# Performance work log

Hardware: AMD Instinct MI355X
Metric: run time of the kernel (lower is better)

The kernel has to match this reference:

```python
import jax, jax.numpy as jnp
import numpy as np

N = 50000
E = 800000
F_IN = 512
HID = 32
HEADS = 8
CLS = 64
NEG_SLOPE = 0.2
EPS = 1e-16  # PyG softmax denominator epsilon


def setup_inputs() -> dict:
    key = jax.random.key(0)
    ks = jax.random.split(key, 10)
    x = jax.random.normal(ks[0], (N, F_IN), dtype=jnp.float32)
    edge_index = jax.random.randint(ks[1], (2, E), 0, N, dtype=jnp.int64)
    # layer 1: in=F_IN, heads=HEADS, out_per_head=HID, concat
    s1 = 1.0 / np.sqrt(F_IN)
    W1 = jax.random.normal(ks[2], (F_IN, HEADS * HID), dtype=jnp.float32) * s1
    att_src1 = jax.random.normal(ks[3], (HEADS, HID), dtype=jnp.float32) * 0.1
    att_dst1 = jax.random.normal(ks[4], (HEADS, HID), dtype=jnp.float32) * 0.1
    b1 = jnp.zeros((HEADS * HID,), dtype=jnp.float32)
    # layer 2: in=HEADS*HID, heads=1, out=CLS, no concat
    s2 = 1.0 / np.sqrt(HEADS * HID)
    W2 = jax.random.normal(ks[5], (HEADS * HID, CLS), dtype=jnp.float32) * s2
    att_src2 = jax.random.normal(ks[6], (1, CLS), dtype=jnp.float32) * 0.1
    att_dst2 = jax.random.normal(ks[7], (1, CLS), dtype=jnp.float32) * 0.1
    b2 = jnp.zeros((CLS,), dtype=jnp.float32)
    return {"x": x, "edge_index": edge_index,
            "W1": W1, "att_src1": att_src1, "att_dst1": att_dst1, "b1": b1,
            "W2": W2, "att_src2": att_src2, "att_dst2": att_dst2, "b2": b2}


def gat_conv(x, edge_index, W, att_src, att_dst, bias, concat):
    n = x.shape[0]
    heads, c = att_src.shape
    h = (x @ W).reshape(n, heads, c)                       # [N,H,C]
    # add self loops (PyG GATConv default)
    loop = jnp.arange(n, dtype=edge_index.dtype)
    src = jnp.concatenate([edge_index[0], loop])
    dst = jnp.concatenate([edge_index[1], loop])
    a_src = jnp.einsum('nhc,hc->nh', h, att_src)           # [N,H]
    a_dst = jnp.einsum('nhc,hc->nh', h, att_dst)
    e = a_src[src] + a_dst[dst]                            # [E',H]
    e = jax.nn.leaky_relu(e, NEG_SLOPE)
    # segment softmax over destination node
    m = jax.ops.segment_max(e, dst, num_segments=n)
    e = jnp.exp(e - jax.lax.stop_gradient(m)[dst])
    s = jax.ops.segment_sum(e, dst, num_segments=n)
    alpha = e / (s[dst] + EPS)                             # [E',H]
    msg = h[src] * alpha[:, :, None]                       # [E',H,C]
    out = jax.ops.segment_sum(msg, dst, num_segments=n)    # [N,H,C]
    out = out.reshape(n, heads * c) if concat else out.mean(axis=1)
    return out + bias


def reference(x, edge_index, W1, att_src1, att_dst1, b1, W2, att_src2, att_dst2, b2):
    h = gat_conv(x, edge_index, W1, att_src1, att_dst1, b1, concat=True)
    h = jax.nn.relu(h)
    # F.dropout with training=False (eval) is identity
    h = gat_conv(h, edge_index, W2, att_src2, att_dst2, b2, concat=False)
    return jax.nn.log_softmax(h, axis=1)
```

## Files before the change

kernel.cpp:

```cpp
#include <hip/hip_runtime.h>
#include <hip/hip_bf16.h>
#include <stdint.h>

#define F_IN 512
#define HID 32
#define HEADS 8
#define C1 (HEADS*HID)
#define CLS 64
#define NEG 0.2f
#define EPS 1e-16f

typedef __bf16 bf16x8 __attribute__((ext_vector_type(8)));
typedef __bf16 bf16x4 __attribute__((ext_vector_type(4)));
typedef float  f32x4  __attribute__((ext_vector_type(4)));

__device__ __forceinline__ float leaky(float v) { return v > 0.f ? v : NEG * v; }

__device__ __forceinline__ bf16x8 cvt8(float4 a, float4 b) {
  bf16x8 o;
  o[0] = (__bf16)a.x; o[1] = (__bf16)a.y; o[2] = (__bf16)a.z; o[3] = (__bf16)a.w;
  o[4] = (__bf16)b.x; o[5] = (__bf16)b.y; o[6] = (__bf16)b.z; o[7] = (__bf16)b.w;
  return o;
}

__global__ __launch_bounds__(256) void prep(const float* __restrict__ W1,
    const float* __restrict__ W2, const int* __restrict__ ei,
    __bf16* __restrict__ w1t, __bf16* __restrict__ w2t,
    int* __restrict__ deg, int E) {
  const int b = blockIdx.x, t = threadIdx.x;
  if (b < 64) {
    int i = b * 256 + t;
    int o0 = i * 8;
    int c = o0 >> 9, k0 = o0 & 511;
    bf16x8 o;
#pragma unroll
    for (int j = 0; j < 8; j++) o[j] = (__bf16)W1[(size_t)(k0 + j) * C1 + c];
    *(bf16x8*)(w1t + (size_t)o0) = o;
  } else if (b < 72) {
    int i = (b - 64) * 256 + t;
    int o0 = i * 8;
    int c = o0 >> 8, k0 = o0 & 255;
    bf16x8 o;
#pragma unroll
    for (int j = 0; j < 8; j++) o[j] = (__bf16)W2[(size_t)(k0 + j) * CLS + c];
    *(bf16x8*)(w2t + (size_t)o0) = o;
  } else {
    int e = (b - 72) * 256 + t;
    if (e < E) atomicAdd(&deg[ei[E + e]], 1);
  }
}

__global__ __launch_bounds__(256) void scan_k1(const int* __restrict__ deg,
    int* __restrict__ bsum, int N) {
  __shared__ int ws[4];
  const int t = threadIdx.x, lane = t & 63, wid = t >> 6;
  int i = blockIdx.x * 256 + t;
  int v = (i < N) ? deg[i] : 0;
#pragma unroll
  for (int o = 1; o < 64; o <<= 1) v += __shfl_xor(v, o);
  if (lane == 0) ws[wid] = v;
  __syncthreads();
  if (t == 0) bsum[blockIdx.x] = ws[0] + ws[1] + ws[2] + ws[3];
}

__global__ __launch_bounds__(256) void scan_k2(int* __restrict__ bsum, int nb) {
  __shared__ int wsum[4];
  __shared__ int carry_s;
  const int t = threadIdx.x, lane = t & 63, wid = t >> 6;
  if (t == 0) carry_s = 0;
  __syncthreads();
  for (int base = 0; base < nb; base += 256) {
    int i = base + t;
    int v = (i < nb) ? bsum[i] : 0;
    int inc = v;
#pragma unroll
    for (int o = 1; o < 64; o <<= 1) { int x = __shfl_up(inc, o); if (lane >= o) inc += x; }
    if (lane == 63) wsum[wid] = inc;
    __syncthreads();
    int woff = 0;
    for (int w = 0; w < wid; w++) woff += wsum[w];
    int excl = carry_s + woff + inc - v;
    if (i < nb) bsum[i] = excl;
    __syncthreads();
    if (t == 0) carry_s += wsum[0] + wsum[1] + wsum[2] + wsum[3];
    __syncthreads();
  }
}

__global__ __launch_bounds__(256) void scan_k3(const int* __restrict__ deg,
    const int* __restrict__ bsum, int* __restrict__ rowstart,
    int* __restrict__ cur, int N) {
  __shared__ int wsum[4];
  const int t = threadIdx.x, lane = t & 63, wid = t >> 6;
  int i = blockIdx.x * 256 + t;
  int v = (i < N) ? deg[i] : 0;
  int inc = v;
#pragma unroll
  for (int o = 1; o < 64; o <<= 1) { int x = __shfl_up(inc, o); if (lane >= o) inc += x; }
  if (lane == 63) wsum[wid] = inc;
  __syncthreads();
  int woff = 0;
  for (int w = 0; w < wid; w++) woff += wsum[w];
  int excl = bsum[blockIdx.x] + woff + inc - v;
  if (i < N) { rowstart[i] = excl; cur[i] = excl; }
  if (i == N - 1) rowstart[N] = excl + v;
}

__global__ __launch_bounds__(256) void scatter_csr(const int* __restrict__ ei,
    int* __restrict__ cur, int* __restrict__ csr_src, int E) {
  int e = blockIdx.x * 256 + threadIdx.x;
  if (e >= E) return;
  int s = ei[e], d = ei[E + e];
  int pos = atomicAdd(&cur[d], 1);
  csr_src[pos] = s;
}

__global__ __launch_bounds__(256) void gemm1_fused(const float* __restrict__ A,
    const __bf16* __restrict__ Bt, __bf16* __restrict__ C,
    const float* __restrict__ asw, const float* __restrict__ adw,
    float* __restrict__ a_src, float* __restrict__ a_dst, int M) {
  __shared__ __bf16 Al[128 * 32];
  __shared__ __bf16 Bl[128 * 32];
  const int tid = threadIdx.x, lane = tid & 63, wave = tid >> 6;
  const int lm = lane & 15, q = lane >> 4;
  const int wr = (wave >> 1) * 64, wc = (wave & 1) * 64;
  const int bm = blockIdx.y * 128, bn = blockIdx.x * 128;
  const int srow = tid >> 2, skc = (tid & 3) * 8;

  f32x4 acc[4][4];
#pragma unroll
  for (int i = 0; i < 4; i++)
#pragma unroll
    for (int j = 0; j < 4; j++) acc[i][j] = (f32x4){0.f, 0.f, 0.f, 0.f};

  const int ra0 = min(bm + srow, M - 1);
  const int ra1 = min(bm + srow + 64, M - 1);
  const int rb0 = bn + srow, rb1 = bn + srow + 64;

  float4 a00, a01, a10, a11;
  bf16x8 vb0, vb1;
  a00 = *(const float4*)(A + (size_t)ra0 * 512 + skc);
  a01 = *(const float4*)(A + (size_t)ra0 * 512 + skc + 4);
  a10 = *(const float4*)(A + (size_t)ra1 * 512 + skc);
  a11 = *(const float4*)(A + (size_t)ra1 * 512 + skc + 4);
  vb0 = *(const bf16x8*)(Bt + (size_t)rb0 * 512 + skc);
  vb1 = *(const bf16x8*)(Bt + (size_t)rb1 * 512 + skc);

  for (int kk = 0; kk < 16; kk++) {
    __syncthreads();
    *(bf16x8*)(Al + srow * 32 + skc)        = cvt8(a00, a01);
    *(bf16x8*)(Al + (srow + 64) * 32 + skc) = cvt8(a10, a11);
    *(bf16x8*)(Bl + srow * 32 + skc)        = vb0;
    *(bf16x8*)(Bl + (srow + 64) * 32 + skc) = vb1;
    __syncthreads();
    if (kk + 1 < 16) {
      const int k0 = (kk + 1) * 32;
      a00 = *(const float4*)(A + (size_t)ra0 * 512 + k0 + skc);
      a01 = *(const float4*)(A + (size_t)ra0 * 512 + k0 + skc + 4);
      a10 = *(const float4*)(A + (size_t)ra1 * 512 + k0 + skc);
      a11 = *(const float4*)(A + (size_t)ra1 * 512 + k0 + skc + 4);
      vb0 = *(const bf16x8*)(Bt + (size_t)rb0 * 512 + k0 + skc);
      vb1 = *(const bf16x8*)(Bt + (size_t)rb1 * 512 + k0 + skc);
    }
    bf16x8 af[4], bfr[4];
#pragma unroll
    for (int mi = 0; mi < 4; mi++)
      af[mi] = *(const bf16x8*)(Al + (wr + mi * 16 + lm) * 32 + q * 8);
#pragma unroll
    for (int ni = 0; ni < 4; ni++)
      bfr[ni] = *(const bf16x8*)(Bl + (wc + ni * 16 + lm) * 32 + q * 8);
#pragma unroll
    for (int mi = 0; mi < 4; mi++)
#pragma unroll
      for (int ni = 0; ni < 4; ni++)
        acc[mi][ni] = __builtin_amdgcn_mfma_f32_16x16x32_bf16(af[mi], bfr[ni], acc[mi][ni], 0, 0, 0);
  }

#pragma unroll
  for (int mi = 0; mi < 4; mi++) {
#pragma unroll
    for (int ni = 0; ni < 4; ni++) {
      const int col = bn + wc + ni * 16 + lm;
#pragma unroll
      for (int r = 0; r < 4; r++) {
        const int row = bm + wr + mi * 16 + q * 4 + r;
        if (row < M) C[(size_t)row * C1 + col] = (__bf16)acc[mi][ni][r];
      }
    }
  }

  {
    const int cb = bn + wc;
    const int h0 = cb >> 5;
    float ws[4], wd[4];
#pragma unroll
    for (int ni = 0; ni < 4; ni++) {
      ws[ni] = asw[cb + ni * 16 + lm];
      wd[ni] = adw[cb + ni * 16 + lm];
    }
#pragma unroll
    for (int mi = 0; mi < 4; mi++) {
#pragma unroll
      for (int r = 0; r < 4; r++) {
        float ps0 = acc[mi][0][r] * ws[0] + acc[mi][1][r] * ws[1];
        float ps1 = acc[mi][2][r] * ws[2] + acc[mi][3][r] * ws[3];
        float pd0 = acc[mi][0][r] * wd[0] + acc[mi][1][r] * wd[1];
        float pd1 = acc[mi][2][r] * wd[2] + acc[mi][3][r] * wd[3];
#pragma unroll
        for (int o = 1; o <= 8; o <<= 1) {
          ps0 += __shfl_xor(ps0, o); ps1 += __shfl_xor(ps1, o);
          pd0 += __shfl_xor(pd0, o); pd1 += __shfl_xor(pd1, o);
        }
        if (lm == 0) {
          const int row = bm + wr + mi * 16 + q * 4 + r;
          if (row < M) {
            a_src[(size_t)row * 8 + h0]     = ps0;
            a_src[(size_t)row * 8 + h0 + 1] = ps1;
            a_dst[(size_t)row * 8 + h0]     = pd0;
            a_dst[(size_t)row * 8 + h0 + 1] = pd1;
          }
        }
      }
    }
  }
}

__global__ __launch_bounds__(256) void gemm2_fused(const __bf16* __restrict__ A,
    const __bf16* __restrict__ Bt, __bf16* __restrict__ C,
    const float* __restrict__ asw, const float* __restrict__ adw,
    float* __restrict__ a_src, float* __restrict__ a_dst, int M) {
  __shared__ __bf16 Al[128 * 32];
  __shared__ __bf16 Bl[64 * 32];
  __shared__ float sred[128][2][2];
  const int tid = threadIdx.x, lane = tid & 63, wave = tid >> 6;
  const int lm = lane & 15, q = lane >> 4;
  const int wr = (wave >> 1) * 64, wc = (wave & 1) * 32;
  const int bm = blockIdx.x * 128;
  const int srow = tid >> 2, skc = (tid & 3) * 8;

  f32x4 acc[4][2];
#pragma unroll
  for (int i = 0; i < 4; i++)
#pragma unroll
    for (int j = 0; j < 2; j++) acc[i][j] = (f32x4){0.f, 0.f, 0.f, 0.f};

  const int ra0 = min(bm + srow, M - 1);
  const int ra1 = min(bm + srow + 64, M - 1);

  bf16x8 va0, va1, vb;
  va0 = *(const bf16x8*)(A + (size_t)ra0 * C1 + skc);
  va1 = *(const bf16x8*)(A + (size_t)ra1 * C1 + skc);
  vb  = *(const bf16x8*)(Bt + (size_t)srow * C1 + skc);

  for (int kk = 0; kk < 8; kk++) {
    __syncthreads();
    *(bf16x8*)(Al + srow * 32 + skc)        = va0;
    *(bf16x8*)(Al + (srow + 64) * 32 + skc) = va1;
    *(bf16x8*)(Bl + srow * 32 + skc)        = vb;
    __syncthreads();
    if (kk + 1 < 8) {
      const int k0 = (kk + 1) * 32;
      va0 = *(const bf16x8*)(A + (size_t)ra0 * C1 + k0 + skc);
      va1 = *(const bf16x8*)(A + (size_t)ra1 * C1 + k0 + skc);
      vb  = *(const bf16x8*)(Bt + (size_t)srow * C1 + k0 + skc);
    }
    bf16x8 af[4], bfr[2];
#pragma unroll
    for (int mi = 0; mi < 4; mi++)
      af[mi] = *(const bf16x8*)(Al + (wr + mi * 16 + lm) * 32 + q * 8);
#pragma unroll
    for (int ni = 0; ni < 2; ni++)
      bfr[ni] = *(const bf16x8*)(Bl + (wc + ni * 16 + lm) * 32 + q * 8);
#pragma unroll
    for (int mi = 0; mi < 4; mi++)
#pragma unroll
      for (int ni = 0; ni < 2; ni++)
        acc[mi][ni] = __builtin_amdgcn_mfma_f32_16x16x32_bf16(af[mi], bfr[ni], acc[mi][ni], 0, 0, 0);
  }

  float ws[2], wd[2];
#pragma unroll
  for (int ni = 0; ni < 2; ni++) {
    ws[ni] = asw[wc + ni * 16 + lm];
    wd[ni] = adw[wc + ni * 16 + lm];
  }
#pragma unroll
  for (int mi = 0; mi < 4; mi++) {
#pragma unroll
    for (int ni = 0; ni < 2; ni++) {
      const int col = wc + ni * 16 + lm;
#pragma unroll
      for (int r = 0; r < 4; r++) {
        const int row = bm + wr + mi * 16 + q * 4 + r;
        if (row < M) C[(size_t)row * CLS + col] = (__bf16)acc[mi][ni][r];
      }
    }
#pragma unroll
    for (int r = 0; r < 4; r++) {
      float ps = acc[mi][0][r] * ws[0] + acc[mi][1][r] * ws[1];
      float pd = acc[mi][0][r] * wd[0] + acc[mi][1][r] * wd[1];
#pragma unroll
      for (int o = 1; o <= 8; o <<= 1) { ps += __shfl_xor(ps, o); pd += __shfl_xor(pd, o); }
      if (lm == 0) {
        const int rl = wr + mi * 16 + q * 4 + r;
        sred[rl][wave & 1][0] = ps;
        sred[rl][wave & 1][1] = pd;
      }
    }
  }
  __syncthreads();
  if (tid < 128) {
    const int row = bm + tid;
    if (row < M) {
      a_src[row] = sred[tid][0][0] + sred[tid][1][0];
      a_dst[row] = sred[tid][0][1] + sred[tid][1][1];
    }
  }
}

__global__ __launch_bounds__(256) void gather1(const int* __restrict__ rowstart,
    const int* __restrict__ csr_src, const __bf16* __restrict__ h1,
    const float* __restrict__ as1, const float* __restrict__ ad1,
    const float* __restrict__ b1, __bf16* __restrict__ o1, int N) {
  const int t = threadIdx.x;
  const int d = blockIdx.x * 4 + (t >> 6);
  if (d >= N) return;
  const int lane = t & 63;
  const int e8 = lane >> 3, hh = lane & 7;
  const int r0 = rowstart[d];
  const int deg = rowstart[d + 1] - r0;

  const float addh = ad1[(uint32_t)d * 8u + hh];
  const float self_e = __expf(leaky(as1[(uint32_t)d * 8u + hh] + addh));

  int   se[8];
  float ex[8];
#pragma unroll
  for (int ch = 0; ch < 8; ch++) {
    const int j = ch * 8 + e8;
    se[ch] = 0; ex[ch] = 0.f;
    if (j < deg) {
      int s = csr_src[r0 + j];
      se[ch] = s;
      ex[ch] = __expf(leaky(as1[(uint32_t)s * 8u + hh] + addh));
    }
  }
  float sum = 0.f;
#pragma unroll
  for (int ch = 0; ch < 8; ch++) sum += ex[ch];
  for (int j0 = 64; j0 < deg; j0 += 8) {
    int j = j0 + e8;
    if (j < deg) {
      int s = csr_src[r0 + j];
      sum += __expf(leaky(as1[(uint32_t)s * 8u + hh] + addh));
    }
  }
  sum += __shfl_xor(sum, 8);
  sum += __shfl_xor(sum, 16);
  sum += __shfl_xor(sum, 32);
  sum += self_e;
  const float inv = 1.f / (sum + EPS);

  float al[8];
#pragma unroll
  for (int ch = 0; ch < 8; ch++) al[ch] = ex[ch] * inv;
  const float al_self_byhh = self_e * inv;

  const int p = lane >> 5, g = lane & 31, hg = g >> 2;
  float acc[8];
#pragma unroll
  for (int i = 0; i < 8; i++) acc[i] = 0.f;

#pragma unroll
  for (int ch = 0; ch < 8; ch++) {
    if (ch * 8 < deg) {
      const int   s0 = __shfl(se[ch], (p + 0) * 8);
      const int   s1 = __shfl(se[ch], (p + 2) * 8);
      const int   s2 = __shfl(se[ch], (p + 4) * 8);
      const int   s3 = __shfl(se[ch], (p + 6) * 8);
      const float a0 = __shfl(al[ch], (p + 0) * 8 + hg);
      const float a1 = __shfl(al[ch], (p + 2) * 8 + hg);
      const float a2 = __shfl(al[ch], (p + 4) * 8 + hg);
      const float a3 = __shfl(al[ch], (p + 6) * 8 + hg);
      bf16x8 x0 = *(const bf16x8*)(h1 + ((uint32_t)s0 * 256u + (uint32_t)(g * 8)));
      bf16x8 x1 = *(const bf16x8*)(h1 + ((uint32_t)s1 * 256u + (uint32_t)(g * 8)));
      bf16x8 x2 = *(const bf16x8*)(h1 + ((uint32_t)s2 * 256u + (uint32_t)(g * 8)));
      bf16x8 x3 = *(const bf16x8*)(h1 + ((uint32_t)s3 * 256u + (uint32_t)(g * 8)));
#pragma unroll
      for (int i = 0; i < 8; i++) acc[i] += a0 * (float)x0[i];
#pragma unroll
      for (int i = 0; i < 8; i++) acc[i] += a1 * (float)x1[i];
#pragma unroll
      for (int i = 0; i < 8; i++) acc[i] += a2 * (float)x2[i];
#pragma unroll
      for (int i = 0; i < 8; i++) acc[i] += a3 * (float)x3[i];
    }
  }
  for (int j0 = 64; j0 < deg; j0 += 8) {
    int j = j0 + e8;
    int se2 = 0; float al2 = 0.f;
    if (j < deg) { se2 = csr_src[r0 + j]; al2 = __expf(leaky(as1[(uint32_t)se2 * 8u + hh] + addh)) * inv; }
#pragma unroll
    for (int it = 0; it < 4; it++) {
      if (j0 + it * 2 < deg) {
        const int   jj  = it * 2 + p;
        const int   s_j = __shfl(se2, jj * 8);
        const float a_j = __shfl(al2, jj * 8 + hg);
        bf16x8 x = *(const bf16x8*)(h1 + ((uint32_t)s_j * 256u + (uint32_t)(g * 8)));
#pragma unroll
        for (int i = 0; i < 8; i++) acc[i] += a_j * (float)x[i];
      }
    }
  }
#pragma unroll
  for (int i = 0; i < 8; i++) acc[i] += __shfl_xor(acc[i], 32);

  const float a_selfh = __shfl(al_self_byhh, hg);
  if (lane < 32) {
    bf16x8 xs = *(const bf16x8*)(h1 + ((uint32_t)d * 256u + (uint32_t)(g * 8)));
    const float4 b4a = *(const float4*)(b1 + g * 8);
    const float4 b4b = *(const float4*)(b1 + g * 8 + 4);
    bf16x8 o;
    o[0] = (__bf16)fmaxf(acc[0] + a_selfh * (float)xs[0] + b4a.x, 0.f);
    o[1] = (__bf16)fmaxf(acc[1] + a_selfh * (float)xs[1] + b4a.y, 0.f);
    o[2] = (__bf16)fmaxf(acc[2] + a_selfh * (float)xs[2] + b4a.z, 0.f);
    o[3] = (__bf16)fmaxf(acc[3] + a_selfh * (float)xs[3] + b4a.w, 0.f);
    o[4] = (__bf16)fmaxf(acc[4] + a_selfh * (float)xs[4] + b4b.x, 0.f);
    o[5] = (__bf16)fmaxf(acc[5] + a_selfh * (float)xs[5] + b4b.y, 0.f);
    o[6] = (__bf16)fmaxf(acc[6] + a_selfh * (float)xs[6] + b4b.z, 0.f);
    o[7] = (__bf16)fmaxf(acc[7] + a_selfh * (float)xs[7] + b4b.w, 0.f);
    *(bf16x8*)(o1 + (uint32_t)d * 256u + (uint32_t)(g * 8)) = o;
  }
}

__global__ __launch_bounds__(256) void gather2(const int* __restrict__ rowstart,
    const int* __restrict__ csr_src, const __bf16* __restrict__ h2b,
    const float* __restrict__ as2, const float* __restrict__ ad2,
    const float* __restrict__ b2, float* __restrict__ out, int N) {
  const int t = threadIdx.x, lane = t & 63;
  const int d = blockIdx.x * 4 + (t >> 6);
  if (d >= N) return;
  const int r0 = rowstart[d], deg = rowstart[d + 1] - r0;
  const float addd = ad2[d];
  const float self_e = __expf(leaky(as2[d] + addd));

  int se = 0; float ex = 0.f;
  if (lane < deg) { se = csr_src[r0 + lane]; ex = __expf(leaky(as2[se] + addd)); }
  float sum = ex;
  for (int j0 = 64; j0 < deg; j0 += 64) {
    int j = j0 + lane;
    if (j < deg) sum += __expf(leaky(as2[csr_src[r0 + j]] + addd));
  }
#pragma unroll
  for (int o = 1; o < 64; o <<= 1) sum += __shfl_xor(sum, o);
  sum += self_e;
  const float inv = 1.f / (sum + EPS);
  const float alpha = ex * inv;
  const float al_self = self_e * inv;

  const int e8 = lane >> 3, c8 = lane & 7;
  float acc[8];
#pragma unroll
  for (int i = 0; i < 8; i++) acc[i] = 0.f;

#pragma unroll
  for (int itg = 0; itg < 8; itg += 2) {
    if (itg * 8 < deg) {
      const int   sa = __shfl(se, itg * 8 + e8);
      const int   sb = __shfl(se, itg * 8 + 8 + e8);
      const float aa = __shfl(alpha, itg * 8 + e8);
      const float ab = __shfl(alpha, itg * 8 + 8 + e8);
      bf16x8 xa = *(const bf16x8*)(h2b + ((uint32_t)sa * 64u + (uint32_t)(c8 * 8)));
      bf16x8 xb = *(const bf16x8*)(h2b + ((uint32_t)sb * 64u + (uint32_t)(c8 * 8)));
#pragma unroll
      for (int i = 0; i < 8; i++) acc[i] += aa * (float)xa[i];
#pragma unroll
      for (int i = 0; i < 8; i++) acc[i] += ab * (float)xb[i];
    }
  }
  for (int j0 = 64; j0 < deg; j0 += 64) {
    int j = j0 + lane;
    int se2 = 0; float al2 = 0.f;
    if (j < deg) { se2 = csr_src[r0 + j]; al2 = __expf(leaky(as2[se2] + addd)) * inv; }
#pragma unroll
    for (int it = 0; it < 8; it++) {
      if (j0 + it * 8 < deg) {
        const int   jj  = it * 8 + e8;
        const int   s_j = __shfl(se2, jj);
        const float a_j = __shfl(al2, jj);
        bf16x8 x = *(const bf16x8*)(h2b + ((uint32_t)s_j * 64u + (uint32_t)(c8 * 8)));
#pragma unroll
        for (int i = 0; i < 8; i++) acc[i] += a_j * (float)x[i];
      }
    }
  }
#pragma unroll
  for (int i = 0; i < 8; i++) {
    acc[i] += __shfl_xor(acc[i], 8);
    acc[i] += __shfl_xor(acc[i], 16);
    acc[i] += __shfl_xor(acc[i], 32);
  }

  bf16x8 xs = *(const bf16x8*)(h2b + ((uint32_t)d * 64u + (uint32_t)(c8 * 8)));
  const float4 bba = *(const float4*)(b2 + c8 * 8);
  const float4 bbb = *(const float4*)(b2 + c8 * 8 + 4);
  float v[8];
  v[0] = acc[0] + al_self * (float)xs[0] + bba.x;
  v[1] = acc[1] + al_self * (float)xs[1] + bba.y;
  v[2] = acc[2] + al_self * (float)xs[2] + bba.z;
  v[3] = acc[3] + al_self * (float)xs[3] + bba.w;
  v[4] = acc[4] + al_self * (float)xs[4] + bbb.x;
  v[5] = acc[5] + al_self * (float)xs[5] + bbb.y;
  v[6] = acc[6] + al_self * (float)xs[6] + bbb.z;
  v[7] = acc[7] + al_self * (float)xs[7] + bbb.w;
  float m2 = v[0];
#pragma unroll
  for (int i = 1; i < 8; i++) m2 = fmaxf(m2, v[i]);
  m2 = fmaxf(m2, __shfl_xor(m2, 1));
  m2 = fmaxf(m2, __shfl_xor(m2, 2));
  m2 = fmaxf(m2, __shfl_xor(m2, 4));
  float sm = 0.f;
#pragma unroll
  for (int i = 0; i < 8; i++) sm += __expf(v[i] - m2);
  sm += __shfl_xor(sm, 1);
  sm += __shfl_xor(sm, 2);
  sm += __shfl_xor(sm, 4);
  const float lg = m2 + __logf(sm);
  if (lane < 8) {
    float4 o0, o1v;
    o0.x  = v[0] - lg; o0.y  = v[1] - lg; o0.z  = v[2] - lg; o0.w  = v[3] - lg;
    o1v.x = v[4] - lg; o1v.y = v[5] - lg; o1v.z = v[6] - lg; o1v.w = v[7] - lg;
    *(float4*)(out + (size_t)d * CLS + c8 * 8)     = o0;
    *(float4*)(out + (size_t)d * CLS + c8 * 8 + 4) = o1v;
  }
}

extern "C" void kernel_launch(void* const* d_in, const int* in_sizes, int n_in,
                              void* d_out, int out_size, void* d_ws, size_t ws_size,
                              hipStream_t stream) {
  const float* x        = (const float*)d_in[0];
  const int*   ei       = (const int*)d_in[1];
  const float* W1       = (const float*)d_in[2];
  const float* att_src1 = (const float*)d_in[3];
  const float* att_dst1 = (const float*)d_in[4];
  const float* b1       = (const float*)d_in[5];
  const float* W2       = (const float*)d_in[6];
  const float* att_src2 = (const float*)d_in[7];
  const float* att_dst2 = (const float*)d_in[8];
  const float* b2       = (const float*)d_in[9];
  float* out = (float*)d_out;

  const int N  = in_sizes[0] / F_IN;
  const int E  = in_sizes[1] / 2;
  const int NB = (N + 255) / 256;

  char* ws = (char*)d_ws;
  size_t off = 0;
  auto alloc = [&](size_t bytes) -> void* {
    void* p = ws + off;
    off += (bytes + 255) & ~(size_t)255;
    return p;
  };
  __bf16* h1  = (__bf16*)alloc((size_t)N * C1 * 2);
  __bf16* o1  = (__bf16*)alloc((size_t)N * C1 * 2);
  float*  as1 = (float*)alloc((size_t)N * HEADS * 4);
  float*  ad1 = (float*)alloc((size_t)N * HEADS * 4);
  __bf16* h2b = (__bf16*)alloc((size_t)N * CLS * 2);
  float*  as2 = (float*)alloc((size_t)N * 4);
  float*  ad2 = (float*)alloc((size_t)N * 4);
  int* deg      = (int*)alloc((size_t)N * 4);
  int* rowstart = (int*)alloc((size_t)(N + 1) * 4);
  int* cur      = (int*)alloc((size_t)N * 4);
  int* csr_src  = (int*)alloc((size_t)E * 4);
  int* bsum     = (int*)alloc((size_t)NB * 4);
  __bf16* w1t = (__bf16*)alloc((size_t)C1 * F_IN * 2);
  __bf16* w2t = (__bf16*)alloc((size_t)CLS * C1 * 2);

  hipMemsetAsync(deg, 0, (size_t)N * 4, stream);
  prep<<<72 + (E + 255) / 256, 256, 0, stream>>>(W1, W2, ei, w1t, w2t, deg, E);

  scan_k1<<<NB, 256, 0, stream>>>(deg, bsum, N);
  scan_k2<<<1, 256, 0, stream>>>(bsum, NB);
  scan_k3<<<NB, 256, 0, stream>>>(deg, bsum, rowstart, cur, N);
  scatter_csr<<<(E + 255) / 256, 256, 0, stream>>>(ei, cur, csr_src, E);

  {
    dim3 g(C1 / 128, (N + 127) / 128);
    gemm1_fused<<<g, 256, 0, stream>>>(x, w1t, h1, att_src1, att_dst1, as1, ad1, N);
  }
  gather1<<<(N + 3) / 4, 256, 0, stream>>>(rowstart, csr_src, h1, as1, ad1, b1, o1, N);

  gemm2_fused<<<(N + 127) / 128, 256, 0, stream>>>(o1, w2t, h2b, att_src2, att_dst2, as2, ad2, N);
  gather2<<<(N + 3) / 4, 256, 0, stream>>>(rowstart, csr_src, h2b, as2, ad2, b2, out, N);
}
```

Before: 408.2 us.

## Pre-convert x to bf16 and double-buffer gemm1 with direct global-to-LDS loads

The prep kernel gains a pass that converts the fp32 input features to bf16 once. gemm1 then reads bf16 through async global_load_lds into double-buffered shared memory, so the register staging, conversion and one barrier per k-step go away. The gather1 first-64-neighbour loop is restructured from four loads per step to one load per two-edge step. The aliasing of the bf16 x buffer and layer-2 buffers saves workspace. The trade-off is an extra full pass over x and less memory-level parallelism in gather1.

```diff
diff --git a/kernel.cpp b/kernel.cpp
--- a/kernel.cpp
+++ b/kernel.cpp
@@ -23,10 +23,15 @@
   return o;
 }
 
+#define GLOAD_LDS16(gsrc, ldst) \
+  __builtin_amdgcn_global_load_lds((const __attribute__((address_space(1))) void*)(gsrc), \
+      (__attribute__((address_space(3))) void*)(ldst), 16, 0, 0)
+
 __global__ __launch_bounds__(256) void prep(const float* __restrict__ W1,
     const float* __restrict__ W2, const int* __restrict__ ei,
-    __bf16* __restrict__ w1t, __bf16* __restrict__ w2t,
-    int* __restrict__ deg, int E) {
+    const float* __restrict__ x, __bf16* __restrict__ w1t,
+    __bf16* __restrict__ w2t, __bf16* __restrict__ xb,
+    int* __restrict__ deg, int E, int EB, int XN) {
   const int b = blockIdx.x, t = threadIdx.x;
   if (b < 64) {
     int i = b * 256 + t;
@@ -44,9 +49,17 @@
 #pragma unroll
     for (int j = 0; j < 8; j++) o[j] = (__bf16)W2[(size_t)(k0 + j) * CLS + c];
     *(bf16x8*)(w2t + (size_t)o0) = o;
-  } else {
+  } else if (b < 72 + EB) {
     int e = (b - 72) * 256 + t;
     if (e < E) atomicAdd(&deg[ei[E + e]], 1);
+  } else {
+    int i = (b - 72 - EB) * 256 + t;
+    int o0 = i * 8;
+    if (o0 < XN) {
+      float4 f0 = *(const float4*)(x + o0);
+      float4 f1 = *(const float4*)(x + o0 + 4);
+      *(bf16x8*)(xb + o0) = cvt8(f0, f1);
+    }
   }
 }
 
@@ -115,12 +128,12 @@
   csr_src[pos] = s;
 }
 
-__global__ __launch_bounds__(256) void gemm1_fused(const float* __restrict__ A,
+__global__ __launch_bounds__(256) void gemm1_fused(const __bf16* __restrict__ A,
     const __bf16* __restrict__ Bt, __bf16* __restrict__ C,
     const float* __restrict__ asw, const float* __restrict__ adw,
     float* __restrict__ a_src, float* __restrict__ a_dst, int M) {
-  __shared__ __bf16 Al[128 * 32];
-  __shared__ __bf16 Bl[128 * 32];
+  __shared__ __bf16 Al[2][128 * 32];
+  __shared__ __bf16 Bl[2][128 * 32];
   const int tid = threadIdx.x, lane = tid & 63, wave = tid >> 6;
   const int lm = lane & 15, q = lane >> 4;
   const int wr = (wave >> 1) * 64, wc = (wave & 1) * 64;
@@ -137,43 +150,44 @@
   const int ra1 = min(bm + srow + 64, M - 1);
   const int rb0 = bn + srow, rb1 = bn + srow + 64;
 
-  float4 a00, a01, a10, a11;
-  bf16x8 vb0, vb1;
-  a00 = *(const float4*)(A + (size_t)ra0 * 512 + skc);
-  a01 = *(const float4*)(A + (size_t)ra0 * 512 + skc + 4);
-  a10 = *(const float4*)(A + (size_t)ra1 * 512 + skc);
-  a11 = *(const float4*)(A + (size_t)ra1 * 512 + skc + 4);
-  vb0 = *(const bf16x8*)(Bt + (size_t)rb0 * 512 + skc);
-  vb1 = *(const bf16x8*)(Bt + (size_t)rb1 * 512 + skc);
-
+  const __bf16* ga0 = A + (size_t)ra0 * 512 + skc;
+  const __bf16* ga1 = A + (size_t)ra1 * 512 + skc;
+  const __bf16* gb0 = Bt + (size_t)rb0 * 512 + skc;
+  const __bf16* gb1 = Bt + (size_t)rb1 * 512 + skc;
+  const int l0 = srow * 32 + skc;
+  const int l1 = (srow + 64) * 32 + skc;
+
+  GLOAD_LDS16(ga0, &Al[0][l0]);
+  GLOAD_LDS16(ga1, &Al[0][l1]);
+  GLOAD_LDS16(gb0, &Bl[0][l0]);
+  GLOAD_LDS16(gb1, &Bl[0][l1]);
+  asm volatile("s_waitcnt vmcnt(0)" ::: "memory");
+  __syncthreads();
+
+  int cur = 0;
   for (int kk = 0; kk < 16; kk++) {
-    __syncthreads();
-    *(bf16x8*)(Al + srow * 32 + skc)        = cvt8(a00, a01);
-    *(bf16x8*)(Al + (srow + 64) * 32 + skc) = cvt8(a10, a11);
-    *(bf16x8*)(Bl + srow * 32 + skc)        = vb0;
-    *(bf16x8*)(Bl + (srow + 64) * 32 + skc) = vb1;
-    __syncthreads();
     if (kk + 1 < 16) {
       const int k0 = (kk + 1) * 32;
-      a00 = *(const float4*)(A + (size_t)ra0 * 512 + k0 + skc);
-      a01 = *(const float4*)(A + (size_t)ra0 * 512 + k0 + skc + 4);
-      a10 = *(const float4*)(A + (size_t)ra1 * 512 + k0 + skc);
-      a11 = *(const float4*)(A + (size_t)ra1 * 512 + k0 + skc + 4);
-      vb0 = *(const bf16x8*)(Bt + (size_t)rb0 * 512 + k0 + skc);
-      vb1 = *(const bf16x8*)(Bt + (size_t)rb1 * 512 + k0 + skc);
+      GLOAD_LDS16(ga0 + k0, &Al[cur ^ 1][l0]);
+      GLOAD_LDS16(ga1 + k0, &Al[cur ^ 1][l1]);
+      GLOAD_LDS16(gb0 + k0, &Bl[cur ^ 1][l0]);
+      GLOAD_LDS16(gb1 + k0, &Bl[cur ^ 1][l1]);
     }
     bf16x8 af[4], bfr[4];
 #pragma unroll
     for (int mi = 0; mi < 4; mi++)
-      af[mi] = *(const bf16x8*)(Al + (wr + mi * 16 + lm) * 32 + q * 8);
+      af[mi] = *(const bf16x8*)(&Al[cur][(wr + mi * 16 + lm) * 32 + q * 8]);
 #pragma unroll
     for (int ni = 0; ni < 4; ni++)
-      bfr[ni] = *(const bf16x8*)(Bl + (wc + ni * 16 + lm) * 32 + q * 8);
+      bfr[ni] = *(const bf16x8*)(&Bl[cur][(wc + ni * 16 + lm) * 32 + q * 8]);
 #pragma unroll
     for (int mi = 0; mi < 4; mi++)
 #pragma unroll
       for (int ni = 0; ni < 4; ni++)
         acc[mi][ni] = __builtin_amdgcn_mfma_f32_16x16x32_bf16(af[mi], bfr[ni], acc[mi][ni], 0, 0, 0);
+    asm volatile("s_waitcnt vmcnt(0)" ::: "memory");
+    __syncthreads();
+    cur ^= 1;
   }
 
 #pragma unroll
@@ -372,28 +386,14 @@
   for (int i = 0; i < 8; i++) acc[i] = 0.f;
 
 #pragma unroll
-  for (int ch = 0; ch < 8; ch++) {
-    if (ch * 8 < deg) {
-      const int   s0 = __shfl(se[ch], (p + 0) * 8);
-      const int   s1 = __shfl(se[ch], (p + 2) * 8);
-      const int   s2 = __shfl(se[ch], (p + 4) * 8);
-      const int   s3 = __shfl(se[ch], (p + 6) * 8);
-      const float a0 = __shfl(al[ch], (p + 0) * 8 + hg);
-      const float a1 = __shfl(al[ch], (p + 2) * 8 + hg);
-      const float a2 = __shfl(al[ch], (p + 4) * 8 + hg);
-      const float a3 = __shfl(al[ch], (p + 6) * 8 + hg);
-      bf16x8 x0 = *(const bf16x8*)(h1 + ((uint32_t)s0 * 256u + (uint32_t)(g * 8)));
-      bf16x8 x1 = *(const bf16x8*)(h1 + ((uint32_t)s1 * 256u + (uint32_t)(g * 8)));
-      bf16x8 x2 = *(const bf16x8*)(h1 + ((uint32_t)s2 * 256u + (uint32_t)(g * 8)));
-      bf16x8 x3 = *(const bf16x8*)(h1 + ((uint32_t)s3 * 256u + (uint32_t)(g * 8)));
-#pragma unroll
-      for (int i = 0; i < 8; i++) acc[i] += a0 * (float)x0[i];
-#pragma unroll
-      for (int i = 0; i < 8; i++) acc[i] += a1 * (float)x1[i];
-#pragma unroll
-      for (int i = 0; i < 8; i++) acc[i] += a2 * (float)x2[i];
-#pragma unroll
-      for (int i = 0; i < 8; i++) acc[i] += a3 * (float)x3[i];
+  for (int it = 0; it < 32; it++) {
+    if (it * 2 < deg) {
+      const int   j   = it * 2 + p;
+      const int   s_j = __shfl(se[it >> 2], (j & 7) * 8);
+      const float a_j = __shfl(al[it >> 2], (j & 7) * 8 + hg);
+      bf16x8 x = *(const bf16x8*)(h1 + (uint32_t)s_j * 256u + (uint32_t)(g * 8));
+#pragma unroll
+      for (int i = 0; i < 8; i++) acc[i] += a_j * (float)x[i];
     }
   }
   for (int j0 = 64; j0 < deg; j0 += 8) {
@@ -406,7 +406,7 @@
         const int   jj  = it * 2 + p;
         const int   s_j = __shfl(se2, jj * 8);
         const float a_j = __shfl(al2, jj * 8 + hg);
-        bf16x8 x = *(const bf16x8*)(h1 + ((uint32_t)s_j * 256u + (uint32_t)(g * 8)));
+        bf16x8 x = *(const bf16x8*)(h1 + (uint32_t)s_j * 256u + (uint32_t)(g * 8));
 #pragma unroll
         for (int i = 0; i < 8; i++) acc[i] += a_j * (float)x[i];
       }
@@ -417,7 +417,7 @@
 
   const float a_selfh = __shfl(al_self_byhh, hg);
   if (lane < 32) {
-    bf16x8 xs = *(const bf16x8*)(h1 + ((uint32_t)d * 256u + (uint32_t)(g * 8)));
+    bf16x8 xs = *(const bf16x8*)(h1 + (uint32_t)d * 256u + (uint32_t)(g * 8));
     const float4 b4a = *(const float4*)(b1 + g * 8);
     const float4 b4b = *(const float4*)(b1 + g * 8 + 4);
     bf16x8 o;
@@ -553,6 +553,9 @@
   const int N  = in_sizes[0] / F_IN;
   const int E  = in_sizes[1] / 2;
   const int NB = (N + 255) / 256;
+  const int EB = (E + 255) / 256;
+  const int XN = N * F_IN;
+  const int XB_BLKS = (XN / 8 + 255) / 256;
 
   char* ws = (char*)d_ws;
   size_t off = 0;
@@ -562,12 +565,8 @@
     return p;
   };
   __bf16* h1  = (__bf16*)alloc((size_t)N * C1 * 2);
-  __bf16* o1  = (__bf16*)alloc((size_t)N * C1 * 2);
   float*  as1 = (float*)alloc((size_t)N * HEADS * 4);
   float*  ad1 = (float*)alloc((size_t)N * HEADS * 4);
-  __bf16* h2b = (__bf16*)alloc((size_t)N * CLS * 2);
-  float*  as2 = (float*)alloc((size_t)N * 4);
-  float*  ad2 = (float*)alloc((size_t)N * 4);
   int* deg      = (int*)alloc((size_t)N * 4);
   int* rowstart = (int*)alloc((size_t)(N + 1) * 4);
   int* cur      = (int*)alloc((size_t)N * 4);
@@ -575,18 +574,24 @@
   int* bsum     = (int*)alloc((size_t)NB * 4);
   __bf16* w1t = (__bf16*)alloc((size_t)C1 * F_IN * 2);
   __bf16* w2t = (__bf16*)alloc((size_t)CLS * C1 * 2);
+  size_t xb_off = off;
+  __bf16* xb  = (__bf16*)alloc((size_t)N * F_IN * 2);
+  __bf16* o1  = (__bf16*)(ws + xb_off);
+  __bf16* h2b = o1 + (size_t)N * C1;
+  float*  as2 = (float*)(h2b + (size_t)N * CLS);
+  float*  ad2 = as2 + N;
 
   hipMemsetAsync(deg, 0, (size_t)N * 4, stream);
-  prep<<<72 + (E + 255) / 256, 256, 0, stream>>>(W1, W2, ei, w1t, w2t, deg, E);
+  prep<<<72 + EB + XB_BLKS, 256, 0, stream>>>(W1, W2, ei, x, w1t, w2t, xb, deg, E, EB, XN);
 
   scan_k1<<<NB, 256, 0, stream>>>(deg, bsum, N);
   scan_k2<<<1, 256, 0, stream>>>(bsum, NB);
   scan_k3<<<NB, 256, 0, stream>>>(deg, bsum, rowstart, cur, N);
-  scatter_csr<<<(E + 255) / 256, 256, 0, stream>>>(ei, cur, csr_src, E);
+  scatter_csr<<<EB, 256, 0, stream>>>(ei, cur, csr_src, E);
 
   {
     dim3 g(C1 / 128, (N + 127) / 128);
-    gemm1_fused<<<g, 256, 0, stream>>>(x, w1t, h1, att_src1, att_dst1, as1, ad1, N);
+    gemm1_fused<<<g, 256, 0, stream>>>(xb, w1t, h1, att_src1, att_dst1, as1, ad1, N);
   }
   gather1<<<(N + 3) / 4, 256, 0, stream>>>(rowstart, csr_src, h1, as1, ad1, b1, o1, N);
 
```

Result: slower. 448.8 us (+9.9%).
